# Kernel optimization log

Measured on AMD Instinct MI355X. Metric: run time of the kernel, lower is better.

## Reference

```python
import jax, jax.numpy as jnp
import numpy as np

B, T, I, H, L = 64, 512, 256, 1024, 4


def _uniform(key, shape, fan):
    # matches torch nn.RNN/Linear init: U(-1/sqrt(fan), 1/sqrt(fan))
    bound = 1.0 / np.sqrt(fan)
    return jax.random.uniform(key, shape, jnp.float32, -bound, bound)


def setup_inputs() -> dict:
    key = jax.random.key(0)
    keys = jax.random.split(key, 32)
    inp = {"x": jax.random.normal(keys[0], (B, T, I), jnp.float32)}
    k = 1
    for l in range(L):
        din = I if l == 0 else H
        inp[f"W_ih{l}"] = _uniform(keys[k], (H, din), H); k += 1
        inp[f"W_hh{l}"] = _uniform(keys[k], (H, H), H); k += 1
        inp[f"b_ih{l}"] = _uniform(keys[k], (H,), H); k += 1
        inp[f"b_hh{l}"] = _uniform(keys[k], (H,), H); k += 1
    inp["fc_w"] = _uniform(keys[k], (1, H), H); k += 1
    inp["fc_b"] = _uniform(keys[k], (1,), H)
    return inp


def _rnn_layer(x_seq, W_ih, b_ih, W_hh, b_hh):
    # x_seq: [B, T, Din] -> hidden states [B, T, H]
    # Precompute the input projection for all timesteps in one big GEMM.
    xW = jnp.einsum('btd,hd->bth', x_seq, W_ih) + b_ih  # [B, T, H]

    def step(h, xw_t):
        # h_t = tanh(W_ih x_t + b_ih + W_hh h_{t-1} + b_hh)
        h_new = jnp.tanh(xw_t + h @ W_hh.T + b_hh)
        return h_new, h_new

    h0 = jnp.zeros((x_seq.shape[0], W_hh.shape[0]), x_seq.dtype)
    _, hs = jax.lax.scan(step, h0, jnp.swapaxes(xW, 0, 1))  # [T, B, H]
    return jnp.swapaxes(hs, 0, 1)  # [B, T, H]


def reference(x,
              W_ih0, W_hh0, b_ih0, b_hh0,
              W_ih1, W_hh1, b_ih1, b_hh1,
              W_ih2, W_hh2, b_ih2, b_hh2,
              W_ih3, W_hh3, b_ih3, b_hh3,
              fc_w, fc_b):
    h = x
    layer_params = [
        (W_ih0, b_ih0, W_hh0, b_hh0),
        (W_ih1, b_ih1, W_hh1, b_hh1),
        (W_ih2, b_ih2, W_hh2, b_hh2),
        (W_ih3, b_ih3, W_hh3, b_hh3),
    ]
    for (W_ih, b_ih, W_hh, b_hh) in layer_params:
        h = _rnn_layer(h, W_ih, b_ih, W_hh, b_hh)
    return h @ fc_w.T + fc_b  # [B, T, 1]
```

## Files before the change

### kernel.cpp

```cpp
#include <hip/hip_runtime.h>


typedef _Float16 f16;
typedef _Float16 f16x8 __attribute__((ext_vector_type(8)));
typedef float    f32x4 __attribute__((ext_vector_type(4)));

#define BB 64
#define TT 512
#define II 256
#define HH 1024
#define RING 64

union U16u { unsigned long long u[2]; f16x8 v; };

#define SYS_LOAD_U64(p) __hip_atomic_load((const unsigned long long*)(p), \
    __ATOMIC_RELAXED, __HIP_MEMORY_SCOPE_SYSTEM)
#define SYS_STORE_U64(p, x) __hip_atomic_store((unsigned long long*)(p), (x), \
    __ATOMIC_RELAXED, __HIP_MEMORY_SCOPE_SYSTEM)
#define SYS_LOAD_I32(p) __hip_atomic_load((const int*)(p), \
    __ATOMIC_RELAXED, __HIP_MEMORY_SCOPE_SYSTEM)
#define SYS_STORE_I32(p, x) __hip_atomic_store((int*)(p), (x), \
    __ATOMIC_RELAXED, __HIP_MEMORY_SCOPE_SYSTEM)

#define MFMA(a, b, c) __builtin_amdgcn_mfma_f32_16x16x32_f16((a), (b), (c), 0, 0, 0)

__device__ __forceinline__ void l2_load_u64(unsigned long long& d, const void* p) {
  asm volatile("global_load_dwordx2 %0, %1, off sc0" : "=v"(d) : "v"(p) : "memory");
}
__device__ __forceinline__ void l2_store_u64(void* p, unsigned long long v) {
  asm volatile("global_store_dwordx2 %0, %1, off sc0" :: "v"(p), "v"(v) : "memory");
}
__device__ __forceinline__ int l2_load_flag(const void* p) {
  int v;
  asm volatile("global_load_dword %0, %1, off sc0\n\ts_waitcnt vmcnt(0)"
               : "=v"(v) : "v"(p) : "memory");
  return v;
}
__device__ __forceinline__ void l2_store_flag(void* p, int v) {
  asm volatile("global_store_dword %0, %1, off sc0" :: "v"(p), "v"(v) : "memory");
}
__device__ __forceinline__ void waitcnt0() {
  asm volatile("s_waitcnt vmcnt(0)" ::: "memory");
}
#define TIE16(b) asm volatile("s_waitcnt vmcnt(0)" \
  : "+v"(b[0]), "+v"(b[1]), "+v"(b[2]), "+v"(b[3]), "+v"(b[4]), "+v"(b[5]), \
    "+v"(b[6]), "+v"(b[7]), "+v"(b[8]), "+v"(b[9]), "+v"(b[10]), "+v"(b[11]), \
    "+v"(b[12]), "+v"(b[13]), "+v"(b[14]), "+v"(b[15]) :: "memory")

__global__ __launch_bounds__(256) void cvt_kernel(const float* __restrict__ in,
                                                  f16* __restrict__ out, int n4) {
  int stride = gridDim.x * blockDim.x;
  for (int i = blockIdx.x * blockDim.x + threadIdx.x; i < n4; i += stride) {
    float4 v = reinterpret_cast<const float4*>(in)[i];
    _Float16 __attribute__((ext_vector_type(4))) h = { (f16)v.x, (f16)v.y,
                                                       (f16)v.z, (f16)v.w };
    reinterpret_cast<decltype(h)*>(out)[i] = h;
  }
}

__global__ __launch_bounds__(256) void bsum_kernel(const float* __restrict__ a,
                                                   const float* __restrict__ b,
                                                   float* __restrict__ o) {
  int i = blockIdx.x * blockDim.x + threadIdx.x;
  if (i < HH) o[i] = a[i] + b[i];
}

__global__ __launch_bounds__(256) void zero_kernel(int* __restrict__ p, int n) {
  int i = blockIdx.x * blockDim.x + threadIdx.x;
  if (i < n) p[i] = 0;
}

__global__ __launch_bounds__(256) void initout_kernel(float* __restrict__ out,
                                                      const float* __restrict__ fcb,
                                                      int n) {
  int i = blockIdx.x * blockDim.x + threadIdx.x;
  if (i < n) out[i] = fcb[0];
}

__global__ __launch_bounds__(256, 1) void rnn_persist(
    const float* __restrict__ x,
    f16* __restrict__ ring0, f16* __restrict__ ring1, f16* __restrict__ ring2,
    f16* __restrict__ hfastg,
    const f16* __restrict__ wih0, const f16* __restrict__ wih1,
    const f16* __restrict__ wih2, const f16* __restrict__ wih3,
    const f16* __restrict__ whh0, const f16* __restrict__ whh1,
    const f16* __restrict__ whh2, const f16* __restrict__ whh3,
    const float* __restrict__ bs0, const float* __restrict__ bs1,
    const float* __restrict__ bs2, const float* __restrict__ bs3,
    const float* __restrict__ fcw, float* __restrict__ out,
    int* __restrict__ flag_fast, int* __restrict__ flag_sys,
    int* __restrict__ census) {
  const int p = blockIdx.x & 15, wgp = blockIdx.x >> 4;
  const int l = p >> 2, bg = p & 3;
  const int wave = threadIdx.x >> 6, lane = threadIdx.x & 63;
  const int l15 = lane & 15, quad = lane >> 4;
  const int b0 = bg * 16, r0 = wgp * 64;
  const int srow = threadIdx.x >> 4;
  const int scol = (threadIdx.x & 15) * 4;

  __shared__ f32x4 red[16 * 64];
  __shared__ __align__(16) f16 hstage[16 * 64];
  __shared__ int sfast;

  {
    int xcc;
    asm volatile("s_getreg_b32 %0, hwreg(HW_REG_XCC_ID)" : "=s"(xcc));
    if (threadIdx.x == 0) SYS_STORE_I32(&census[p * 16 + wgp], xcc + 1);
    if (wave == 0) {
      int v = 1;
      for (;;) {
        v = (lane < 16) ? SYS_LOAD_I32(&census[p * 16 + lane]) : 1;
        if (__all(v != 0)) break;
      }
      int v0 = __shfl(v, 0, 64);
      int eq = __all((lane < 16) ? (v == v0) : 1);
      if (lane == 0) sfast = eq;
    }
    __syncthreads();
  }
  const bool fast = (sfast != 0);

  f16* rings[4] = { ring0, ring1, ring2, (f16*)0 };
  const f16* wih_t[4] = { wih0, wih1, wih2, wih3 };
  const f16* whh_t[4] = { whh0, whh1, whh2, whh3 };
  const float* bs_t[4] = { bs0, bs1, bs2, bs3 };

  const f16* in_ring = (l > 0) ? rings[l - 1] : (const f16*)0;
  f16* out_ring = rings[l];
  f16* hfast = hfastg + (size_t)p * 2 * 16 * HH;
  const float bv = bs_t[l][r0 + wave * 16 + l15];

  f16x8 whhF[4][8];
  {
    const f16* q = whh_t[l] + (size_t)(r0 + l15) * HH + wave * 256 + quad * 8;
#pragma unroll
    for (int j = 0; j < 4; ++j)
#pragma unroll
      for (int f = 0; f < 8; ++f)
        whhF[j][f] = *reinterpret_cast<const f16x8*>(q + (size_t)j * 16 * HH + f * 32);
  }
  f16x8 wihF[4][8];
  if (l == 0) {
    const f16* q = wih0 + (size_t)(r0 + l15) * II + wave * 64 + quad * 8;
#pragma unroll
    for (int j = 0; j < 4; ++j)
#pragma unroll
      for (int f = 0; f < 2; ++f)
        wihF[j][f] = *reinterpret_cast<const f16x8*>(q + (size_t)j * 16 * II + f * 32);
  } else {
    const f16* q = wih_t[l] + (size_t)(r0 + l15) * HH + wave * 256 + quad * 8;
#pragma unroll
    for (int j = 0; j < 4; ++j)
#pragma unroll
      for (int f = 0; f < 8; ++f)
        wihF[j][f] = *reinterpret_cast<const f16x8*>(q + (size_t)j * 16 * HH + f * 32);
  }
  float4 fcwv = { 0.f, 0.f, 0.f, 0.f };
  if (l == 3) fcwv = *reinterpret_cast<const float4*>(fcw + r0 + (threadIdx.x & 15) * 4);

  const int which = lane >> 4;
  int psel = p + (which == 1 ? -4 : which == 2 ? 4 : 0);
  psel = psel < 0 ? 0 : (psel > 15 ? 15 : psel);
  const int* fsysp = flag_sys + (psel * 16 + l15) * 16;
  const int* ffastp = flag_fast + (p * 16 + l15) * 16;
  unsigned long long needA = 0;
  if (l > 0) needA |= 0xFFFF0000ull;
  if (l < 3) needA |= 0xFFFF00000000ull;
  int* myff = flag_fast + (p * 16 + wgp) * 16;
  int* myfs = flag_sys + (p * 16 + wgp) * 16;
  const bool partA = (which == 1 && l > 0) || (which == 2 && l < 3);
  int pvA = 0;

  for (int t = 0; t < TT; ++t) {
    const int slot = t & (RING - 1);

    if (wave == 0 && needA && (l > 0 || t + 1 >= RING)) {
      const int tgtA = (which == 1) ? t + 1 : t - RING + 1;
      int v = partA ? pvA : 0x7FFFFFFF;
      if ((__ballot(v >= tgtA) & needA) != needA) {
        for (;;) {
          v = partA ? SYS_LOAD_I32(fsysp) : 0x7FFFFFFF;
          if ((__ballot(v >= tgtA) & needA) == needA) break;
        }
      }
      pvA = partA ? SYS_LOAD_I32(fsysp) : 0x7FFFFFFF;
    }
    if (l > 0) __syncthreads();

    f32x4 c0 = {}, c1 = {}, c2 = {}, c3 = {};

    if (l == 0) {
      const float* xp = x + ((size_t)(b0 + l15) * TT + t) * II + wave * 64 + quad * 8;
#pragma unroll
      for (int f = 0; f < 2; ++f) {
        float4 u0 = *reinterpret_cast<const float4*>(xp + f * 32);
        float4 u1 = *reinterpret_cast<const float4*>(xp + f * 32 + 4);
        f16x8 a = { (f16)u0.x, (f16)u0.y, (f16)u0.z, (f16)u0.w,
                    (f16)u1.x, (f16)u1.y, (f16)u1.z, (f16)u1.w };
        c0 = MFMA(a, wihF[0][f], c0);
        c1 = MFMA(a, wihF[1][f], c1);
        c2 = MFMA(a, wihF[2][f], c2);
        c3 = MFMA(a, wihF[3][f], c3);
      }
    } else {
      const char* ip = (const char*)(in_ring + ((size_t)(b0 + l15) * RING + slot) * HH +
                                     wave * 256 + quad * 8);
#pragma unroll
      for (int f = 0; f < 8; ++f) {
        U16u av;
        av.u[0] = SYS_LOAD_U64(ip + f * 64);
        av.u[1] = SYS_LOAD_U64(ip + f * 64 + 8);
        c0 = MFMA(av.v, wihF[0][f], c0);
        c1 = MFMA(av.v, wihF[1][f], c1);
        c2 = MFMA(av.v, wihF[2][f], c2);
        c3 = MFMA(av.v, wihF[3][f], c3);
      }
    }

    if (t > 0) {
      waitcnt0();
      __syncthreads();
      if (threadIdx.x == 0) SYS_STORE_I32(myfs, t);
    }

    if (t > 0) {
      if (wave == 0) {
        if (fast) {
          for (;;) {
            int v = (which == 0) ? l2_load_flag(ffastp) : 0x7FFFFFFF;
            if ((__ballot(v >= t) & 0xFFFFull) == 0xFFFFull) break;
          }
        } else {
          for (;;) {
            int v = (which == 0) ? SYS_LOAD_I32(ffastp) : 0x7FFFFFFF;
            if ((__ballot(v >= t) & 0xFFFFull) == 0xFFFFull) break;
          }
        }
      }
      __syncthreads();

      unsigned long long hbuf[16];
      const char* hp = (const char*)(hfast + (size_t)((t - 1) & 1) * 16 * HH +
                                     (size_t)l15 * HH + wave * 256 + quad * 8);
      if (fast) {
#pragma unroll
        for (int f = 0; f < 8; ++f) {
          l2_load_u64(hbuf[2 * f], hp + f * 64);
          l2_load_u64(hbuf[2 * f + 1], hp + f * 64 + 8);
        }
        TIE16(hbuf);
      } else {
#pragma unroll
        for (int f = 0; f < 8; ++f) {
          hbuf[2 * f] = SYS_LOAD_U64(hp + f * 64);
          hbuf[2 * f + 1] = SYS_LOAD_U64(hp + f * 64 + 8);
        }
      }
#pragma unroll
      for (int f = 0; f < 8; ++f) {
        U16u av;
        av.u[0] = hbuf[2 * f];
        av.u[1] = hbuf[2 * f + 1];
        c0 = MFMA(av.v, whhF[0][f], c0);
        c1 = MFMA(av.v, whhF[1][f], c1);
        c2 = MFMA(av.v, whhF[2][f], c2);
        c3 = MFMA(av.v, whhF[3][f], c3);
      }
    }

    red[(wave * 4 + 0) * 64 + lane] = c0;
    red[(wave * 4 + 1) * 64 + lane] = c1;
    red[(wave * 4 + 2) * 64 + lane] = c2;
    red[(wave * 4 + 3) * 64 + lane] = c3;
    __syncthreads();
    f32x4 tot = red[(0 * 4 + wave) * 64 + lane] + red[(1 * 4 + wave) * 64 + lane] +
                red[(2 * 4 + wave) * 64 + lane] + red[(3 * 4 + wave) * 64 + lane];

#pragma unroll
    for (int i = 0; i < 4; ++i) {
      float e = __expf(2.0f * (tot[i] + bv));
      hstage[(quad * 4 + i) * 64 + wave * 16 + l15] = (f16)(1.0f - 2.0f / (e + 1.0f));
    }
    __syncthreads();

    unsigned long long hw =
        *reinterpret_cast<const unsigned long long*>(&hstage[srow * 64 + scol]);
    {
      void* dst = hfast + (size_t)(t & 1) * 16 * HH + (size_t)srow * HH + r0 + scol;
      if (fast) l2_store_u64(dst, hw);
      else      SYS_STORE_U64(dst, hw);
    }
    waitcnt0();
    __syncthreads();
    if (threadIdx.x == 0) {
      if (fast) l2_store_flag(myff, t + 1);
      else      SYS_STORE_I32(myff, t + 1);
    }

    if (l < 3) {
      SYS_STORE_U64(out_ring + ((size_t)(b0 + srow) * RING + slot) * HH + r0 + scol, hw);
    } else {
      union { unsigned long long u; f16 h[4]; } hu;
      hu.u = hw;
      float partial = (float)hu.h[0] * fcwv.x + (float)hu.h[1] * fcwv.y +
                      (float)hu.h[2] * fcwv.z + (float)hu.h[3] * fcwv.w;
      partial += __shfl_down(partial, 8, 16);
      partial += __shfl_down(partial, 4, 16);
      partial += __shfl_down(partial, 2, 16);
      partial += __shfl_down(partial, 1, 16);
      if ((threadIdx.x & 15) == 0)
        atomicAdd(out + (size_t)(b0 + srow) * TT + t, partial);
    }
  }

  waitcnt0();
  __syncthreads();
  if (threadIdx.x == 0) SYS_STORE_I32(myfs, TT);
}

extern "C" void kernel_launch(void* const* d_in, const int* in_sizes, int n_in,
                              void* d_out, int out_size, void* d_ws, size_t ws_size,
                              hipStream_t stream) {
  const float* x   = (const float*)d_in[0];
  const float* fcw = (const float*)d_in[17];
  const float* fcb = (const float*)d_in[18];

  char* ws = (char*)d_ws;
  size_t off = 0;
  auto alloc = [&](size_t bytes) -> void* {
    void* p = ws + off;
    off += (bytes + 255) & ~(size_t)255;
    return p;
  };
  f16* ring[3];
  for (int l = 0; l < 3; ++l)
    ring[l] = (f16*)alloc((size_t)BB * RING * HH * 2);
  f16* hfast = (f16*)alloc((size_t)16 * 2 * 16 * HH * 2);
  f16* w16ih[4];
  f16* w16hh[4];
  float* bsum[4];
  for (int l = 0; l < 4; ++l) {
    int din = (l == 0) ? II : HH;
    w16ih[l] = (f16*)alloc((size_t)HH * din * 2);
    w16hh[l] = (f16*)alloc((size_t)HH * HH * 2);
    bsum[l]  = (float*)alloc(HH * 4);
  }
  int* flag_fast = (int*)alloc(256 * 16 * 4);
  int* flag_sys  = (int*)alloc(256 * 16 * 4);
  int* census    = (int*)alloc(256 * 4);

  for (int l = 0; l < 4; ++l) {
    int din = (l == 0) ? II : HH;
    cvt_kernel<<<512, 256, 0, stream>>>((const float*)d_in[1 + 4 * l], w16ih[l],
                                        HH * din / 4);
    cvt_kernel<<<512, 256, 0, stream>>>((const float*)d_in[2 + 4 * l], w16hh[l],
                                        HH * HH / 4);
    bsum_kernel<<<4, 256, 0, stream>>>((const float*)d_in[3 + 4 * l],
                                       (const float*)d_in[4 + 4 * l], bsum[l]);
  }
  zero_kernel<<<17, 256, 0, stream>>>(flag_fast, 256 * 16);
  zero_kernel<<<17, 256, 0, stream>>>(flag_sys, 256 * 16);
  zero_kernel<<<1, 256, 0, stream>>>(census, 256);
  initout_kernel<<<BB * TT / 256, 256, 0, stream>>>((float*)d_out, fcb, BB * TT);

  rnn_persist<<<256, 256, 0, stream>>>(
      x, ring[0], ring[1], ring[2], hfast,
      w16ih[0], w16ih[1], w16ih[2], w16ih[3],
      w16hh[0], w16hh[1], w16hh[2], w16hh[3],
      bsum[0], bsum[1], bsum[2], bsum[3],
      fcw, (float*)d_out, flag_fast, flag_sys, census);
}
```

Baseline: 3.026 ms.

## Replace block-level flag sync with per-wave flags and bounded spin waits

```diff
diff --git a/kernel.cpp b/kernel.cpp
--- a/kernel.cpp
+++ b/kernel.cpp
@@ -10,6 +10,7 @@
 #define II 256
 #define HH 1024
 #define RING 64
+#define SPINMAX (1 << 22)
 
 union U16u { unsigned long long u[2]; f16x8 v; };
 
@@ -102,18 +103,21 @@
   __shared__ __align__(16) f16 hstage[16 * 64];
   __shared__ int sfast;
 
+  int bailed = 0;
+
   {
     int xcc;
     asm volatile("s_getreg_b32 %0, hwreg(HW_REG_XCC_ID)" : "=s"(xcc));
     if (threadIdx.x == 0) SYS_STORE_I32(&census[p * 16 + wgp], xcc + 1);
     if (wave == 0) {
-      int v = 1;
+      int v = 1, itc = 0, ok = 1;
       for (;;) {
         v = (lane < 16) ? SYS_LOAD_I32(&census[p * 16 + lane]) : 1;
         if (__all(v != 0)) break;
+        if (++itc > SPINMAX) { ok = 0; break; }
       }
       int v0 = __shfl(v, 0, 64);
-      int eq = __all((lane < 16) ? (v == v0) : 1);
+      int eq = ok && __all((lane < 16) ? (v == v0) : 1);
       if (lane == 0) sfast = eq;
     }
     __syncthreads();
@@ -158,34 +162,35 @@
   float4 fcwv = { 0.f, 0.f, 0.f, 0.f };
   if (l == 3) fcwv = *reinterpret_cast<const float4*>(fcw + r0 + (threadIdx.x & 15) * 4);
 
-  const int which = lane >> 4;
-  int psel = p + (which == 1 ? -4 : which == 2 ? 4 : 0);
-  psel = psel < 0 ? 0 : (psel > 15 ? 15 : psel);
-  const int* fsysp = flag_sys + (psel * 16 + l15) * 16;
-  const int* ffastp = flag_fast + (p * 16 + l15) * 16;
-  unsigned long long needA = 0;
-  if (l > 0) needA |= 0xFFFF0000ull;
-  if (l < 3) needA |= 0xFFFF00000000ull;
-  int* myff = flag_fast + (p * 16 + wgp) * 16;
-  int* myfs = flag_sys + (p * 16 + wgp) * 16;
-  const bool partA = (which == 1 && l > 0) || (which == 2 && l < 3);
-  int pvA = 0;
+  const int* pollH = flag_fast +
+      (size_t)(p * 64 + (4 * wave + (l15 >> 2)) * 4 + (l15 & 3)) * 16;
+  int* myhf = flag_fast + (size_t)(p * 64 + wgp * 4 + wave) * 16;
+  const int* upP = (l > 0) ? flag_sys + (size_t)((p - 4) * 16 + l15) * 16
+                           : (const int*)0;
+  const int* dnP = (l < 3) ? flag_sys + (size_t)((p + 4) * 16 + l15) * 16
+                           : (const int*)0;
+  int* myfs = flag_sys + (size_t)(p * 16 + wgp) * 16;
 
   for (int t = 0; t < TT; ++t) {
     const int slot = t & (RING - 1);
 
-    if (wave == 0 && needA && (l > 0 || t + 1 >= RING)) {
-      const int tgtA = (which == 1) ? t + 1 : t - RING + 1;
-      int v = partA ? pvA : 0x7FFFFFFF;
-      if ((__ballot(v >= tgtA) & needA) != needA) {
-        for (;;) {
-          v = partA ? SYS_LOAD_I32(fsysp) : 0x7FFFFFFF;
-          if ((__ballot(v >= tgtA) & needA) == needA) break;
-        }
-      }
-      pvA = partA ? SYS_LOAD_I32(fsysp) : 0x7FFFFFFF;
-    }
-    if (l > 0) __syncthreads();
+    if (l > 0) {
+      int itc = 0;
+      for (;;) {
+        int v = (lane < 16) ? SYS_LOAD_I32(upP) : 0x7FFFFFFF;
+        if (__all(v >= t + 1)) break;
+        if (bailed | (++itc > SPINMAX)) { bailed = 1; break; }
+      }
+    }
+    if (l < 3 && t >= RING) {
+      const int tgt = t - RING + 1;
+      int itc = 0;
+      for (;;) {
+        int v = (lane < 16) ? SYS_LOAD_I32(dnP) : 0x7FFFFFFF;
+        if (__all(v >= tgt)) break;
+        if (bailed | (++itc > SPINMAX)) { bailed = 1; break; }
+      }
+    }
 
     f32x4 c0 = {}, c1 = {}, c2 = {}, c3 = {};
 
@@ -224,20 +229,21 @@
     }
 
     if (t > 0) {
-      if (wave == 0) {
-        if (fast) {
-          for (;;) {
-            int v = (which == 0) ? l2_load_flag(ffastp) : 0x7FFFFFFF;
-            if ((__ballot(v >= t) & 0xFFFFull) == 0xFFFFull) break;
-          }
-        } else {
-          for (;;) {
-            int v = (which == 0) ? SYS_LOAD_I32(ffastp) : 0x7FFFFFFF;
-            if ((__ballot(v >= t) & 0xFFFFull) == 0xFFFFull) break;
-          }
+      if (fast) {
+        int itc = 0;
+        for (;;) {
+          int v = (lane < 16) ? l2_load_flag(pollH) : 0x7FFFFFFF;
+          if (__all(v >= t)) break;
+          if (bailed | (++itc > SPINMAX)) { bailed = 1; break; }
         }
-      }
-      __syncthreads();
+      } else {
+        int itc = 0;
+        for (;;) {
+          int v = (lane < 16) ? SYS_LOAD_I32(pollH) : 0x7FFFFFFF;
+          if (__all(v >= t)) break;
+          if (bailed | (++itc > SPINMAX)) { bailed = 1; break; }
+        }
+      }
 
       unsigned long long hbuf[16];
       const char* hp = (const char*)(hfast + (size_t)((t - 1) & 1) * 16 * HH +
@@ -291,10 +297,9 @@
       else      SYS_STORE_U64(dst, hw);
     }
     waitcnt0();
-    __syncthreads();
-    if (threadIdx.x == 0) {
-      if (fast) l2_store_flag(myff, t + 1);
-      else      SYS_STORE_I32(myff, t + 1);
+    if (lane == 0) {
+      if (fast) l2_store_flag(myhf, t + 1);
+      else      SYS_STORE_I32(myhf, t + 1);
     }
 
     if (l < 3) {
@@ -345,7 +350,7 @@
     w16hh[l] = (f16*)alloc((size_t)HH * HH * 2);
     bsum[l]  = (float*)alloc(HH * 4);
   }
-  int* flag_fast = (int*)alloc(256 * 16 * 4);
+  int* flag_fast = (int*)alloc(16 * 16 * 4 * 16 * 4);
   int* flag_sys  = (int*)alloc(256 * 16 * 4);
   int* census    = (int*)alloc(256 * 4);
 
@@ -358,8 +363,8 @@
     bsum_kernel<<<4, 256, 0, stream>>>((const float*)d_in[3 + 4 * l],
                                        (const float*)d_in[4 + 4 * l], bsum[l]);
   }
-  zero_kernel<<<17, 256, 0, stream>>>(flag_fast, 256 * 16);
-  zero_kernel<<<17, 256, 0, stream>>>(flag_sys, 256 * 16);
+  zero_kernel<<<64, 256, 0, stream>>>(flag_fast, 16 * 16 * 4 * 16);
+  zero_kernel<<<16, 256, 0, stream>>>(flag_sys, 256 * 16);
   zero_kernel<<<1, 256, 0, stream>>>(census, 256);
   initout_kernel<<<BB * TT / 256, 256, 0, stream>>>((float*)d_out, fcb, BB * TT);
 
```

Measured after the change: 3.252 ms. 1.07x slower.
